# Kernel tuning notes

Measured on AMD Instinct MI355X. Metric: run time of the kernel, lower is better.

The kernel has to match this reference:

```python
import jax, jax.numpy as jnp
import numpy as np

M, N, D, P = 16, 4096, 128, 8192
H = N // D


def setup_inputs() -> dict:
    key = jax.random.key(0)
    ks = jax.random.split(key, 6)
    return {
        "X": jax.random.normal(ks[0], (M, N), dtype=jnp.float32),
        "W_q": jax.random.normal(ks[1], (N, N), dtype=jnp.float32) / np.sqrt(N),
        "W_k": jax.random.normal(ks[2], (N, N), dtype=jnp.float32) / np.sqrt(N),
        "W_v": jax.random.normal(ks[3], (N, N), dtype=jnp.float32) / np.sqrt(N),
        "cache_K": jax.random.normal(ks[4], (H, P, D), dtype=jnp.float32),
        "cache_V": jax.random.normal(ks[5], (H, P, D), dtype=jnp.float32),
    }


def _rms(x):
    # unaffine RMS norm over last dim, no eps (matches torch source)
    return x * jax.lax.rsqrt(jnp.mean(jnp.square(x), axis=-1, keepdims=True))


def reference(X, W_q, W_k, W_v, cache_K, cache_V):
    m, n = X.shape
    h, p, d = cache_K.shape
    # QKV projections -> [H, M, D]
    q = (X @ W_q).reshape(m, h, d).swapaxes(0, 1)
    k = (X @ W_k).reshape(m, h, d).swapaxes(0, 1)
    v = (X @ W_v).reshape(m, h, d).swapaxes(0, 1)
    q_norm = _rms(q)
    k_norm = _rms(k)
    # prepend KV cache: [H, P+M, D]
    k_cache = jnp.concatenate([cache_K[:, :p, :], k_norm], axis=1)
    v_cache = jnp.concatenate([cache_V[:, :p, :], v], axis=1)
    # attention WITHOUT 1/sqrt(D) scaling (matches torch source)
    scores = jnp.einsum("hmd,hpd->hmp", q_norm, k_cache)
    weights = jax.nn.softmax(scores, axis=-1)
    out = jnp.einsum("hmp,hpd->hmd", weights, v_cache)  # [H, M, D]
    return out.swapaxes(0, 1).reshape(m, n)
```

## Files before the change

### kernel.cpp

```cpp
#include <hip/hip_runtime.h>
#include <hip/hip_bf16.h>
#include <math.h>

#define M_ 16
#define N_ 4096
#define D_ 128
#define P_ 8192
#define H_ 32

#define NIC 32
#define ICH (N_/NIC)
#define NCB 16

#define CHUNK 64
#define NCH (P_/CHUNK)
#define NCH1 (NCH+1)

#define QKV_SZ       (3*H_*M_*D_)
#define PART_OFF     (QKV_SZ)
#define OPART_OFF    (QKV_SZ)
#define OPART_HALFSZ ((H_*NCH1*M_*D_)/2)
#define ML_OFF       (OPART_OFF + OPART_HALFSZ)

__global__ __launch_bounds__(256) void k_proj(const float* __restrict__ X,
                                              const float* __restrict__ Wq,
                                              const float* __restrict__ Wk,
                                              const float* __restrict__ Wv,
                                              float* __restrict__ part) {
  const int mat = blockIdx.z;
  const float* __restrict__ W = (mat == 0) ? Wq : ((mat == 1) ? Wk : Wv);
  const int cb = blockIdx.x, ic = blockIdx.y;
  const int t = threadIdx.x;
  const int j0 = cb * 256 + t;
  const int i0 = ic * ICH;

  __shared__ __align__(16) float XT[ICH][20];

  {
    const int i_l = t & 127, mh = t >> 7;
#pragma unroll
    for (int r = 0; r < 8; ++r)
      XT[i_l][mh * 8 + r] = X[(size_t)(mh * 8 + r) * N_ + i0 + i_l];
  }
  __syncthreads();

  float acc[16];
#pragma unroll
  for (int m = 0; m < 16; ++m) acc[m] = 0.f;

#pragma unroll 8
  for (int i = 0; i < ICH; ++i) {
    const float wv = __builtin_nontemporal_load(W + (size_t)(i0 + i) * N_ + j0);
    float xr[16];
    {
      float4 xv;
      xv = *reinterpret_cast<const float4*>(&XT[i][0]);
      xr[0] = xv.x; xr[1] = xv.y; xr[2] = xv.z; xr[3] = xv.w;
      xv = *reinterpret_cast<const float4*>(&XT[i][4]);
      xr[4] = xv.x; xr[5] = xv.y; xr[6] = xv.z; xr[7] = xv.w;
      xv = *reinterpret_cast<const float4*>(&XT[i][8]);
      xr[8] = xv.x; xr[9] = xv.y; xr[10] = xv.z; xr[11] = xv.w;
      xv = *reinterpret_cast<const float4*>(&XT[i][12]);
      xr[12] = xv.x; xr[13] = xv.y; xr[14] = xv.z; xr[15] = xv.w;
    }
#pragma unroll
    for (int m = 0; m < 16; ++m) acc[m] = fmaf(xr[m], wv, acc[m]);
  }

#pragma unroll
  for (int m = 0; m < 16; ++m)
    __builtin_nontemporal_store(acc[m], part + (size_t)((mat * NIC + ic) * M_ + m) * N_ + j0);
}

__global__ __launch_bounds__(256) void k_reduce(const float* __restrict__ part,
                                                float* __restrict__ qkv) {
  const int mat = blockIdx.z, m = blockIdx.y, nc = blockIdx.x;
  const int t = threadIdx.x;
  const int n = nc * 256 + t;

  float s = 0.f;
#pragma unroll
  for (int ic = 0; ic < NIC; ++ic)
    s += __builtin_nontemporal_load(part + (size_t)((mat * NIC + ic) * M_ + m) * N_ + n);

  float ss = s * s;
#pragma unroll
  for (int off = 1; off < 64; off <<= 1) ss += __shfl_xor(ss, off);
  __shared__ float wsum[4];
  const int wave = t >> 6, lane = t & 63;
  if (lane == 0) wsum[wave] = ss;
  __syncthreads();
  const int half = t >> 7;
  const float tot = wsum[half * 2] + wsum[half * 2 + 1];
  const float scale = (mat < 2) ? rsqrtf(tot * (1.0f / 128.0f)) : 1.0f;

  const int h = n >> 7, d = n & 127;
  qkv[(size_t)((mat * H_ + h) * M_ + m) * D_ + d] = s * scale;
}

__device__ __forceinline__ float fold8(float a[8], int dq) {
#pragma unroll
  for (int i = 0; i < 4; ++i) {
    const float send = (dq & 4) ? a[i] : a[i + 4];
    const float recv = __shfl_xor(send, 4);
    a[i] = ((dq & 4) ? a[i + 4] : a[i]) + recv;
  }
#pragma unroll
  for (int i = 0; i < 2; ++i) {
    const float send = (dq & 2) ? a[i] : a[i + 2];
    const float recv = __shfl_xor(send, 2);
    a[i] = ((dq & 2) ? a[i + 2] : a[i]) + recv;
  }
  {
    const float send = (dq & 1) ? a[0] : a[1];
    const float recv = __shfl_xor(send, 1);
    a[0] = ((dq & 1) ? a[1] : a[0]) + recv;
  }
  return a[0];
}

__device__ __forceinline__ unsigned pk2(float a, float b) {
  __hip_bfloat16 ha = __float2bfloat16(a), hb = __float2bfloat16(b);
  const unsigned short ua = *reinterpret_cast<unsigned short*>(&ha);
  const unsigned short ub = *reinterpret_cast<unsigned short*>(&hb);
  return (unsigned)ua | ((unsigned)ub << 16);
}

__global__ __launch_bounds__(256, 2) void k_attn(const float* __restrict__ cacheK,
                                                 const float* __restrict__ cacheV,
                                                 const float* __restrict__ qkv,
                                                 __hip_bfloat16* __restrict__ opart,
                                                 float* __restrict__ ml) {
  const int c = blockIdx.x, h = blockIdx.y;
  const int t = threadIdx.x;
  const int wave = t >> 6, lane = t & 63;
  const int valid = (c < NCH) ? CHUNK : M_;
  const float* __restrict__ Ksrc = (c < NCH)
      ? (cacheK + ((size_t)h * P_ + (size_t)c * CHUNK) * D_)
      : (qkv + (size_t)((1 * H_ + h) * M_) * D_);
  const float* __restrict__ Vsrc = (c < NCH)
      ? (cacheV + ((size_t)h * P_ + (size_t)c * CHUNK) * D_)
      : (qkv + (size_t)((2 * H_ + h) * M_) * D_);

  __shared__ __align__(16) float smem[4096];
  __shared__ __align__(16) float wx[4 * 128];
  __shared__ __align__(16) float mlx[4][8][2];

  float* qs = smem;
  float* wxp = wx + wave * 128;

  {
    const float4* src = reinterpret_cast<const float4*>(qkv + (size_t)(h * M_) * D_);
    reinterpret_cast<float4*>(qs)[t] = src[t];
    reinterpret_cast<float4*>(qs)[t + 256] = src[t + 256];
  }
  __syncthreads();

  const int pg = lane >> 3, dq = lane & 7;
  const int dl = lane * 2;
  const int rg = wave >> 1, mbase = (wave & 1) * 8;
  const int rbase = rg * 32;
  int rc = valid - rbase; rc = (rc < 0) ? 0 : ((rc > 32) ? 32 : rc);
  const int nb = rc >> 4;

  float mrun = -3.0e38f, lrun = 0.f;
  float2 o[8];
#pragma unroll
  for (int mi = 0; mi < 8; ++mi) o[mi] = make_float2(0.f, 0.f);

  float4 kk[8];
  if (nb > 0) {
    const float* ka = Ksrc + (size_t)(rbase + pg) * D_ + dq * 4;
    kk[0] = *reinterpret_cast<const float4*>(ka);
    kk[1] = *reinterpret_cast<const float4*>(ka + 32);
    kk[2] = *reinterpret_cast<const float4*>(ka + 64);
    kk[3] = *reinterpret_cast<const float4*>(ka + 96);
    const float* kb = Ksrc + (size_t)(rbase + 8 + pg) * D_ + dq * 4;
    kk[4] = *reinterpret_cast<const float4*>(kb);
    kk[5] = *reinterpret_cast<const float4*>(kb + 32);
    kk[6] = *reinterpret_cast<const float4*>(kb + 64);
    kk[7] = *reinterpret_cast<const float4*>(kb + 96);
  }

#pragma unroll 1
  for (int b = 0; b < nb; ++b) {
    const int r0 = rbase + b * 16;

    float2 vvA[8], vvB[8];
#pragma unroll
    for (int j = 0; j < 8; ++j)
      vvA[j] = *reinterpret_cast<const float2*>(Vsrc + (size_t)(r0 + j) * D_ + dl);
#pragma unroll
    for (int j = 0; j < 8; ++j)
      vvB[j] = *reinterpret_cast<const float2*>(Vsrc + (size_t)(r0 + 8 + j) * D_ + dl);

    float aA[8], aB[8];
#pragma unroll
    for (int mi = 0; mi < 8; ++mi) {
      const float* qrow = qs + (mbase + mi) * D_ + dq * 4;
      const float4 q0 = *reinterpret_cast<const float4*>(qrow);
      const float4 q1 = *reinterpret_cast<const float4*>(qrow + 32);
      const float4 q2 = *reinterpret_cast<const float4*>(qrow + 64);
      const float4 q3 = *reinterpret_cast<const float4*>(qrow + 96);
      float sa, sb;
      sa = q0.x * kk[0].x;
      sa = fmaf(q0.y, kk[0].y, sa); sa = fmaf(q0.z, kk[0].z, sa); sa = fmaf(q0.w, kk[0].w, sa);
      sa = fmaf(q1.x, kk[1].x, sa); sa = fmaf(q1.y, kk[1].y, sa);
      sa = fmaf(q1.z, kk[1].z, sa); sa = fmaf(q1.w, kk[1].w, sa);
      sa = fmaf(q2.x, kk[2].x, sa); sa = fmaf(q2.y, kk[2].y, sa);
      sa = fmaf(q2.z, kk[2].z, sa); sa = fmaf(q2.w, kk[2].w, sa);
      sa = fmaf(q3.x, kk[3].x, sa); sa = fmaf(q3.y, kk[3].y, sa);
      sa = fmaf(q3.z, kk[3].z, sa); sa = fmaf(q3.w, kk[3].w, sa);
      sb = q0.x * kk[4].x;
      sb = fmaf(q0.y, kk[4].y, sb); sb = fmaf(q0.z, kk[4].z, sb); sb = fmaf(q0.w, kk[4].w, sb);
      sb = fmaf(q1.x, kk[5].x, sb); sb = fmaf(q1.y, kk[5].y, sb);
      sb = fmaf(q1.z, kk[5].z, sb); sb = fmaf(q1.w, kk[5].w, sb);
      sb = fmaf(q2.x, kk[6].x, sb); sb = fmaf(q2.y, kk[6].y, sb);
      sb = fmaf(q2.z, kk[6].z, sb); sb = fmaf(q2.w, kk[6].w, sb);
      sb = fmaf(q3.x, kk[7].x, sb); sb = fmaf(q3.y, kk[7].y, sb);
      sb = fmaf(q3.z, kk[7].z, sb); sb = fmaf(q3.w, kk[7].w, sb);
      aA[mi] = sa; aB[mi] = sb;
      __builtin_amdgcn_sched_barrier(0);
    }

    {
      int rn = r0 + 16 + pg;
      rn = (rn < valid) ? rn : (valid - 1);
      const float* ka = Ksrc + (size_t)rn * D_ + dq * 4;
      kk[0] = *reinterpret_cast<const float4*>(ka);
      kk[1] = *reinterpret_cast<const float4*>(ka + 32);
      kk[2] = *reinterpret_cast<const float4*>(ka + 64);
      kk[3] = *reinterpret_cast<const float4*>(ka + 96);
      int rn2 = r0 + 24 + pg;
      rn2 = (rn2 < valid) ? rn2 : (valid - 1);
      const float* kb = Ksrc + (size_t)rn2 * D_ + dq * 4;
      kk[4] = *reinterpret_cast<const float4*>(kb);
      kk[5] = *reinterpret_cast<const float4*>(kb + 32);
      kk[6] = *reinterpret_cast<const float4*>(kb + 64);
      kk[7] = *reinterpret_cast<const float4*>(kb + 96);
    }

    const float sA = fold8(aA, dq);
    const float sB = fold8(aB, dq);
    float tmax = fmaxf(sA, sB);
    tmax = fmaxf(tmax, __shfl_xor(tmax, 8));
    tmax = fmaxf(tmax, __shfl_xor(tmax, 16));
    tmax = fmaxf(tmax, __shfl_xor(tmax, 32));
    const float mnew = fmaxf(mrun, tmax);
    const float fc = __expf(mrun - mnew);
    mrun = mnew;
    const float wA = __expf(sA - mnew);
    const float wB = __expf(sB - mnew);
    float rs = wA + wB;
    rs += __shfl_xor(rs, 8); rs += __shfl_xor(rs, 16); rs += __shfl_xor(rs, 32);
    lrun = lrun * fc + rs;

    wxp[pg * 8 + dq] = wA;
    wxp[(8 + pg) * 8 + dq] = wB;

#pragma unroll
    for (int mi = 0; mi < 8; ++mi) {
      const float fcm = __shfl(fc, (lane & 56) | mi);
      o[mi].x *= fcm; o[mi].y *= fcm;
    }

#pragma unroll
    for (int j = 0; j < 8; ++j) {
      const float4 w0 = *reinterpret_cast<const float4*>(&wxp[j * 8]);
      const float4 w1 = *reinterpret_cast<const float4*>(&wxp[j * 8 + 4]);
      const float2 v = vvA[j];
#define PVM(i, wc) o[i].x = fmaf(wc, v.x, o[i].x); o[i].y = fmaf(wc, v.y, o[i].y);
      PVM(0, w0.x) PVM(1, w0.y) PVM(2, w0.z) PVM(3, w0.w)
      PVM(4, w1.x) PVM(5, w1.y) PVM(6, w1.z) PVM(7, w1.w)
#undef PVM
      if (j & 1) __builtin_amdgcn_sched_barrier(0);
    }
#pragma unroll
    for (int j = 0; j < 8; ++j) {
      const float4 w0 = *reinterpret_cast<const float4*>(&wxp[(8 + j) * 8]);
      const float4 w1 = *reinterpret_cast<const float4*>(&wxp[(8 + j) * 8 + 4]);
      const float2 v = vvB[j];
#define PVM(i, wc) o[i].x = fmaf(wc, v.x, o[i].x); o[i].y = fmaf(wc, v.y, o[i].y);
      PVM(0, w0.x) PVM(1, w0.y) PVM(2, w0.z) PVM(3, w0.w)
      PVM(4, w1.x) PVM(5, w1.y) PVM(6, w1.z) PVM(7, w1.w)
#undef PVM
      if (j & 1) __builtin_amdgcn_sched_barrier(0);
    }
  }

  __syncthreads();
  float* obuf = smem;
#pragma unroll
  for (int mi = 0; mi < 8; ++mi)
    *reinterpret_cast<float2*>(&obuf[wave * 1024 + mi * 128 + dl]) = o[mi];
  if (lane < 8) { mlx[wave][lane][0] = mrun; mlx[wave][lane][1] = lrun; }
  __syncthreads();

  {
    const int mm = t >> 4, seg = t & 15;
    const int mh = mm >> 3, mi = mm & 7;
    const float m0v = mlx[mh][mi][0], m1v = mlx[2 + mh][mi][0];
    const float mstar = fmaxf(m0v, m1v);
    const float e0 = __expf(m0v - mstar), e1 = __expf(m1v - mstar);
    const float T = mlx[mh][mi][1] * e0 + mlx[2 + mh][mi][1] * e1;
    const float4 a0 = *reinterpret_cast<const float4*>(&obuf[mh * 1024 + mi * 128 + seg * 8]);
    const float4 a1 = *reinterpret_cast<const float4*>(&obuf[mh * 1024 + mi * 128 + seg * 8 + 4]);
    const float4 b0 = *reinterpret_cast<const float4*>(&obuf[(2 + mh) * 1024 + mi * 128 + seg * 8]);
    const float4 b1 = *reinterpret_cast<const float4*>(&obuf[(2 + mh) * 1024 + mi * 128 + seg * 8 + 4]);
    float r0 = e0 * a0.x + e1 * b0.x, r1 = e0 * a0.y + e1 * b0.y;
    float r2 = e0 * a0.z + e1 * b0.z, r3 = e0 * a0.w + e1 * b0.w;
    float r4 = e0 * a1.x + e1 * b1.x, r5 = e0 * a1.y + e1 * b1.y;
    float r6 = e0 * a1.z + e1 * b1.z, r7 = e0 * a1.w + e1 * b1.w;
    uint4 pk;
    pk.x = pk2(r0, r1); pk.y = pk2(r2, r3); pk.z = pk2(r4, r5); pk.w = pk2(r6, r7);
    const size_t base = ((size_t)(h * NCH1 + c) * M_ + mm) * D_ + seg * 8;
    *reinterpret_cast<uint4*>(opart + base) = pk;
    if (seg == 0) {
      ml[((size_t)(h * NCH1 + c) * M_ + mm) * 2 + 0] = mstar;
      ml[((size_t)(h * NCH1 + c) * M_ + mm) * 2 + 1] = T;
    }
  }
}

__global__ __launch_bounds__(128) void k_comb(const __hip_bfloat16* __restrict__ opart,
                                              const float* __restrict__ ml,
                                              float* __restrict__ out) {
  const int m = blockIdx.x, h = blockIdx.y, t = threadIdx.x;
  __shared__ float Ms[NCH1], Ls[NCH1];
  for (int i = t; i < NCH1; i += 128) {
    Ms[i] = ml[((size_t)(h * NCH1 + i) * M_ + m) * 2 + 0];
    Ls[i] = ml[((size_t)(h * NCH1 + i) * M_ + m) * 2 + 1];
  }
  __syncthreads();
  float gM = -3.0e38f;
#pragma unroll 8
  for (int c2 = 0; c2 < NCH1; ++c2) gM = fmaxf(gM, Ms[c2]);

  const __hip_bfloat16* __restrict__ ob =
      opart + (size_t)h * NCH1 * M_ * D_ + (size_t)m * D_ + t;
  float T = 0.f, o0 = 0.f, o1 = 0.f, o2 = 0.f, o3 = 0.f;
#pragma unroll 4
  for (int c2 = 0; c2 < NCH1 - 1; c2 += 4) {
    const float f0 = __expf(Ms[c2 + 0] - gM);
    const float f1 = __expf(Ms[c2 + 1] - gM);
    const float f2 = __expf(Ms[c2 + 2] - gM);
    const float f3 = __expf(Ms[c2 + 3] - gM);
    T = fmaf(Ls[c2 + 0], f0, T); T = fmaf(Ls[c2 + 1], f1, T);
    T = fmaf(Ls[c2 + 2], f2, T); T = fmaf(Ls[c2 + 3], f3, T);
    o0 = fmaf(__bfloat162float(ob[(size_t)(c2 + 0) * M_ * D_]), f0, o0);
    o1 = fmaf(__bfloat162float(ob[(size_t)(c2 + 1) * M_ * D_]), f1, o1);
    o2 = fmaf(__bfloat162float(ob[(size_t)(c2 + 2) * M_ * D_]), f2, o2);
    o3 = fmaf(__bfloat162float(ob[(size_t)(c2 + 3) * M_ * D_]), f3, o3);
  }
  {
    const int c2 = NCH1 - 1;
    const float f = __expf(Ms[c2] - gM);
    T = fmaf(Ls[c2], f, T);
    o0 = fmaf(__bfloat162float(ob[(size_t)c2 * M_ * D_]), f, o0);
  }
  out[(size_t)m * N_ + h * D_ + t] = (o0 + o1 + o2 + o3) / T;
}

extern "C" void kernel_launch(void* const* d_in, const int* in_sizes, int n_in,
                              void* d_out, int out_size, void* d_ws, size_t ws_size,
                              hipStream_t stream) {
  const float* X  = (const float*)d_in[0];
  const float* Wq = (const float*)d_in[1];
  const float* Wk = (const float*)d_in[2];
  const float* Wv = (const float*)d_in[3];
  const float* cK = (const float*)d_in[4];
  const float* cV = (const float*)d_in[5];
  float* ws    = (float*)d_ws;
  float* qkv   = ws;
  float* part  = ws + PART_OFF;
  __hip_bfloat16* opart = (__hip_bfloat16*)(ws + OPART_OFF);
  float* mlbuf = ws + ML_OFF;
  float* out   = (float*)d_out;

  hipLaunchKernelGGL(k_proj,   dim3(NCB, NIC, 3), dim3(256), 0, stream, X, Wq, Wk, Wv, part);
  hipLaunchKernelGGL(k_reduce, dim3(16, M_, 3),   dim3(256), 0, stream, part, qkv);
  hipLaunchKernelGGL(k_attn,   dim3(NCH1, H_),    dim3(256), 0, stream, cK, cV, qkv, opart, mlbuf);
  hipLaunchKernelGGL(k_comb,   dim3(M_, H_),      dim3(128), 0, stream, opart, mlbuf, out);
}
```

Baseline: 133.0 us.

## Shrink attention inner step to 8 rows and drop K prefetch for higher occupancy

The attention kernel now handles 8 key/value rows per iteration instead of 16. It drops the register-held K prefetch for the next block and loads K at the top of each iteration. Launch bounds change to request 4-8 waves per EU, so the smaller register footprint can raise occupancy and hide memory latency. The cost is more loop iterations, more softmax reduction and shuffle overhead per row, and loss of explicit software prefetch.

```diff
diff --git a/kernel.cpp b/kernel.cpp
--- a/kernel.cpp
+++ b/kernel.cpp
@@ -126,11 +126,12 @@
   return (unsigned)ua | ((unsigned)ub << 16);
 }
 
-__global__ __launch_bounds__(256, 2) void k_attn(const float* __restrict__ cacheK,
-                                                 const float* __restrict__ cacheV,
-                                                 const float* __restrict__ qkv,
-                                                 __hip_bfloat16* __restrict__ opart,
-                                                 float* __restrict__ ml) {
+__global__ __attribute__((amdgpu_waves_per_eu(4, 8)))
+__launch_bounds__(256) void k_attn(const float* __restrict__ cacheK,
+                                   const float* __restrict__ cacheV,
+                                   const float* __restrict__ qkv,
+                                   __hip_bfloat16* __restrict__ opart,
+                                   float* __restrict__ ml) {
   const int c = blockIdx.x, h = blockIdx.y;
   const int t = threadIdx.x;
   const int wave = t >> 6, lane = t & 63;
@@ -161,40 +162,31 @@
   const int rg = wave >> 1, mbase = (wave & 1) * 8;
   const int rbase = rg * 32;
   int rc = valid - rbase; rc = (rc < 0) ? 0 : ((rc > 32) ? 32 : rc);
-  const int nb = rc >> 4;
+  const int nb = rc >> 3;
 
   float mrun = -3.0e38f, lrun = 0.f;
   float2 o[8];
 #pragma unroll
   for (int mi = 0; mi < 8; ++mi) o[mi] = make_float2(0.f, 0.f);
 
-  float4 kk[8];
-  if (nb > 0) {
-    const float* ka = Ksrc + (size_t)(rbase + pg) * D_ + dq * 4;
-    kk[0] = *reinterpret_cast<const float4*>(ka);
-    kk[1] = *reinterpret_cast<const float4*>(ka + 32);
-    kk[2] = *reinterpret_cast<const float4*>(ka + 64);
-    kk[3] = *reinterpret_cast<const float4*>(ka + 96);
-    const float* kb = Ksrc + (size_t)(rbase + 8 + pg) * D_ + dq * 4;
-    kk[4] = *reinterpret_cast<const float4*>(kb);
-    kk[5] = *reinterpret_cast<const float4*>(kb + 32);
-    kk[6] = *reinterpret_cast<const float4*>(kb + 64);
-    kk[7] = *reinterpret_cast<const float4*>(kb + 96);
-  }
-
 #pragma unroll 1
   for (int b = 0; b < nb; ++b) {
-    const int r0 = rbase + b * 16;
-
-    float2 vvA[8], vvB[8];
+    const int r0 = rbase + b * 8;
+
+    float4 kk0, kk1, kk2, kk3;
+    {
+      const float* ka = Ksrc + (size_t)(r0 + pg) * D_ + dq * 4;
+      kk0 = *reinterpret_cast<const float4*>(ka);
+      kk1 = *reinterpret_cast<const float4*>(ka + 32);
+      kk2 = *reinterpret_cast<const float4*>(ka + 64);
+      kk3 = *reinterpret_cast<const float4*>(ka + 96);
+    }
+    float2 vv[8];
 #pragma unroll
     for (int j = 0; j < 8; ++j)
-      vvA[j] = *reinterpret_cast<const float2*>(Vsrc + (size_t)(r0 + j) * D_ + dl);
-#pragma unroll
-    for (int j = 0; j < 8; ++j)
-      vvB[j] = *reinterpret_cast<const float2*>(Vsrc + (size_t)(r0 + 8 + j) * D_ + dl);
-
-    float aA[8], aB[8];
+      vv[j] = *reinterpret_cast<const float2*>(Vsrc + (size_t)(r0 + j) * D_ + dl);
+
+    float a[8];
 #pragma unroll
     for (int mi = 0; mi < 8; ++mi) {
       const float* qrow = qs + (mbase + mi) * D_ + dq * 4;
@@ -202,47 +194,21 @@
       const float4 q1 = *reinterpret_cast<const float4*>(qrow + 32);
       const float4 q2 = *reinterpret_cast<const float4*>(qrow + 64);
       const float4 q3 = *reinterpret_cast<const float4*>(qrow + 96);
-      float sa, sb;
-      sa = q0.x * kk[0].x;
-      sa = fmaf(q0.y, kk[0].y, sa); sa = fmaf(q0.z, kk[0].z, sa); sa = fmaf(q0.w, kk[0].w, sa);
-      sa = fmaf(q1.x, kk[1].x, sa); sa = fmaf(q1.y, kk[1].y, sa);
-      sa = fmaf(q1.z, kk[1].z, sa); sa = fmaf(q1.w, kk[1].w, sa);
-      sa = fmaf(q2.x, kk[2].x, sa); sa = fmaf(q2.y, kk[2].y, sa);
-      sa = fmaf(q2.z, kk[2].z, sa); sa = fmaf(q2.w, kk[2].w, sa);
-      sa = fmaf(q3.x, kk[3].x, sa); sa = fmaf(q3.y, kk[3].y, sa);
-      sa = fmaf(q3.z, kk[3].z, sa); sa = fmaf(q3.w, kk[3].w, sa);
-      sb = q0.x * kk[4].x;
-      sb = fmaf(q0.y, kk[4].y, sb); sb = fmaf(q0.z, kk[4].z, sb); sb = fmaf(q0.w, kk[4].w, sb);
-      sb = fmaf(q1.x, kk[5].x, sb); sb = fmaf(q1.y, kk[5].y, sb);
-      sb = fmaf(q1.z, kk[5].z, sb); sb = fmaf(q1.w, kk[5].w, sb);
-      sb = fmaf(q2.x, kk[6].x, sb); sb = fmaf(q2.y, kk[6].y, sb);
-      sb = fmaf(q2.z, kk[6].z, sb); sb = fmaf(q2.w, kk[6].w, sb);
-      sb = fmaf(q3.x, kk[7].x, sb); sb = fmaf(q3.y, kk[7].y, sb);
-      sb = fmaf(q3.z, kk[7].z, sb); sb = fmaf(q3.w, kk[7].w, sb);
-      aA[mi] = sa; aB[mi] = sb;
+      float s;
+      s = q0.x * kk0.x;
+      s = fmaf(q0.y, kk0.y, s); s = fmaf(q0.z, kk0.z, s); s = fmaf(q0.w, kk0.w, s);
+      s = fmaf(q1.x, kk1.x, s); s = fmaf(q1.y, kk1.y, s);
+      s = fmaf(q1.z, kk1.z, s); s = fmaf(q1.w, kk1.w, s);
+      s = fmaf(q2.x, kk2.x, s); s = fmaf(q2.y, kk2.y, s);
+      s = fmaf(q2.z, kk2.z, s); s = fmaf(q2.w, kk2.w, s);
+      s = fmaf(q3.x, kk3.x, s); s = fmaf(q3.y, kk3.y, s);
+      s = fmaf(q3.z, kk3.z, s); s = fmaf(q3.w, kk3.w, s);
+      a[mi] = s;
       __builtin_amdgcn_sched_barrier(0);
     }
 
-    {
-      int rn = r0 + 16 + pg;
-      rn = (rn < valid) ? rn : (valid - 1);
-      const float* ka = Ksrc + (size_t)rn * D_ + dq * 4;
-      kk[0] = *reinterpret_cast<const float4*>(ka);
-      kk[1] = *reinterpret_cast<const float4*>(ka + 32);
-      kk[2] = *reinterpret_cast<const float4*>(ka + 64);
-      kk[3] = *reinterpret_cast<const float4*>(ka + 96);
-      int rn2 = r0 + 24 + pg;
-      rn2 = (rn2 < valid) ? rn2 : (valid - 1);
-      const float* kb = Ksrc + (size_t)rn2 * D_ + dq * 4;
-      kk[4] = *reinterpret_cast<const float4*>(kb);
-      kk[5] = *reinterpret_cast<const float4*>(kb + 32);
-      kk[6] = *reinterpret_cast<const float4*>(kb + 64);
-      kk[7] = *reinterpret_cast<const float4*>(kb + 96);
-    }
-
-    const float sA = fold8(aA, dq);
-    const float sB = fold8(aB, dq);
-    float tmax = fmaxf(sA, sB);
+    const float sA = fold8(a, dq);
+    float tmax = sA;
     tmax = fmaxf(tmax, __shfl_xor(tmax, 8));
     tmax = fmaxf(tmax, __shfl_xor(tmax, 16));
     tmax = fmaxf(tmax, __shfl_xor(tmax, 32));
@@ -250,13 +216,11 @@
     const float fc = __expf(mrun - mnew);
     mrun = mnew;
     const float wA = __expf(sA - mnew);
-    const float wB = __expf(sB - mnew);
-    float rs = wA + wB;
+    float rs = wA;
     rs += __shfl_xor(rs, 8); rs += __shfl_xor(rs, 16); rs += __shfl_xor(rs, 32);
     lrun = lrun * fc + rs;
 
     wxp[pg * 8 + dq] = wA;
-    wxp[(8 + pg) * 8 + dq] = wB;
 
 #pragma unroll
     for (int mi = 0; mi < 8; ++mi) {
@@ -268,18 +232,7 @@
     for (int j = 0; j < 8; ++j) {
       const float4 w0 = *reinterpret_cast<const float4*>(&wxp[j * 8]);
       const float4 w1 = *reinterpret_cast<const float4*>(&wxp[j * 8 + 4]);
-      const float2 v = vvA[j];
-#define PVM(i, wc) o[i].x = fmaf(wc, v.x, o[i].x); o[i].y = fmaf(wc, v.y, o[i].y);
-      PVM(0, w0.x) PVM(1, w0.y) PVM(2, w0.z) PVM(3, w0.w)
-      PVM(4, w1.x) PVM(5, w1.y) PVM(6, w1.z) PVM(7, w1.w)
-#undef PVM
-      if (j & 1) __builtin_amdgcn_sched_barrier(0);
-    }
-#pragma unroll
-    for (int j = 0; j < 8; ++j) {
-      const float4 w0 = *reinterpret_cast<const float4*>(&wxp[(8 + j) * 8]);
-      const float4 w1 = *reinterpret_cast<const float4*>(&wxp[(8 + j) * 8 + 4]);
-      const float2 v = vvB[j];
+      const float2 v = vv[j];
 #define PVM(i, wc) o[i].x = fmaf(wc, v.x, o[i].x); o[i].y = fmaf(wc, v.y, o[i].y);
       PVM(0, w0.x) PVM(1, w0.y) PVM(2, w0.z) PVM(3, w0.w)
       PVM(4, w1.x) PVM(5, w1.y) PVM(6, w1.z) PVM(7, w1.w)
```

Result: faster. 124.4 us (-6.5%).
